# Performance work log

Hardware: AMD Instinct MI355X
Metric: run time of the kernel (lower is better)

The kernel has to match this reference:

```python
import jax, jax.numpy as jnp
import numpy as np

B, T, H, V = 128, 256, 1024, 4096


def setup_inputs() -> dict:
    key = jax.random.key(0)
    ks = jax.random.split(key, 11)
    s = 1.0 / np.sqrt(H)  # PyTorch default RNN/Linear init scale

    def u(k, shape):
        return jax.random.uniform(k, shape, jnp.float32, -s, s)

    return {
        "x": jax.random.normal(ks[0], (B, 1, T), jnp.float32),
        "W_ih0": u(ks[1], (H, 1)),
        "W_hh0": u(ks[2], (H, H)),
        "b_ih0": u(ks[3], (H,)),
        "b_hh0": u(ks[4], (H,)),
        "W_ih1": u(ks[5], (H, H)),
        "W_hh1": u(ks[6], (H, H)),
        "b_ih1": u(ks[7], (H,)),
        "b_hh1": u(ks[8], (H,)),
        "W_fc": u(ks[9], (V, H)),
        "b_fc": u(ks[10], (V,)),
        "text_length": B,
    }


def reference(x, W_ih0, W_hh0, b_ih0, b_hh0, W_ih1, W_hh1, b_ih1, b_hh1, W_fc, b_fc, text_length):
    # x: [B, 1, T] -> per-step scalar inputs xs: [T, B, 1]
    xs = jnp.transpose(x[:, 0, :], (1, 0))[:, :, None]
    h0 = jnp.zeros((text_length, W_hh0.shape[0]), x.dtype)
    h1 = jnp.zeros_like(h0)

    def step(carry, xt):
        h0, h1 = carry
        # 2-layer Elman RNN cell (tanh), one timestep
        h0n = jnp.tanh(xt @ W_ih0.T + b_ih0 + h0 @ W_hh0.T + b_hh0)
        h1n = jnp.tanh(h0n @ W_ih1.T + b_ih1 + h1 @ W_hh1.T + b_hh1)
        out = h1n @ W_fc.T + b_fc  # fused trailing linear, [B, V]
        return (h0n, h1n), out

    (h0, h1), outs = jax.lax.scan(step, (h0, h1), xs)  # outs: [T, B, V]
    # original returns cat over time then permute(1,0,2) -> [B, T, V]
    return jnp.transpose(outs, (1, 0, 2)), jnp.stack([h0, h1], axis=0)
```

## Files before the change

### kernel.cpp

```cpp
#include <hip/hip_runtime.h>

#define T_STEPS 256
#define BATCH   128
#define HDIM    1024
#define VDIM    4096
#define BH      (BATCH * HDIM)

typedef _Float16 half8 __attribute__((ext_vector_type(8)));
typedef _Float16 half4 __attribute__((ext_vector_type(4)));
typedef float    floatx4 __attribute__((ext_vector_type(4)));

__device__ __forceinline__ half8 ld_h8(const _Float16* p) { return *(const half8*)p; }

__device__ __forceinline__ void async16(void* l, const void* g) {
  __builtin_amdgcn_global_load_lds(
      (const __attribute__((address_space(1))) unsigned int*)g,
      (__attribute__((address_space(3))) unsigned int*)l, 16, 0, 0);
}

__device__ __forceinline__ void wait_ge(unsigned* f, unsigned tgt) {
  while (__hip_atomic_load(f, __ATOMIC_RELAXED, __HIP_MEMORY_SCOPE_AGENT) < tgt)
    __builtin_amdgcn_s_sleep(2);
  (void)__hip_atomic_load(f, __ATOMIC_ACQUIRE, __HIP_MEMORY_SCOPE_AGENT);
}
__device__ __forceinline__ void signal_inc(unsigned* f) {
  __hip_atomic_fetch_add(f, 1u, __ATOMIC_RELEASE, __HIP_MEMORY_SCOPE_AGENT);
}

__device__ __forceinline__ half8 lds_frag(const char* base, int row, int w) {
  return *(const half8*)(base + row * 2048 + ((w ^ (row & 7)) << 4));
}

__global__ __launch_bounds__(256) void f32_to_f16_kernel(
    const float* __restrict__ in, _Float16* __restrict__ out, int n4) {
  int i = blockIdx.x * 256 + threadIdx.x;
  if (i < n4) {
    float4 v = ((const float4*)in)[i];
    half4 h;
    h[0] = (_Float16)v.x; h[1] = (_Float16)v.y;
    h[2] = (_Float16)v.z; h[3] = (_Float16)v.w;
    ((half4*)out)[i] = h;
  }
}

__global__ __launch_bounds__(256, 1) void rnn_kernel(
    const float* __restrict__ x,
    const float* __restrict__ Wih0,
    const float* __restrict__ bih0, const float* __restrict__ bhh0,
    const float* __restrict__ bih1, const float* __restrict__ bhh1,
    const _Float16* __restrict__ W0h,
    const _Float16* __restrict__ W1i,
    const _Float16* __restrict__ W1h,
    _Float16* __restrict__ h0buf,
    _Float16* __restrict__ h1h,
    float* __restrict__ outh,
    unsigned* __restrict__ cnt0,
    unsigned* __restrict__ cnt1) {
  __shared__ __align__(16) char smem[65536];
  const int tid  = threadIdx.x;
  const int wv   = tid >> 6;
  const int lane = tid & 63;
  const int l15  = lane & 15;
  const int q    = lane >> 4;

  const int bid   = blockIdx.x;
  const int layer = bid >> 7;
  const int sub   = bid & 127;
  const int rg    = sub & 7;
  const int cg    = sub >> 3;
  const int rowbase = rg * 16;
  const int j     = cg * 64 + wv * 16 + l15;
  const int qe    = q * 8;

  if (layer == 0) {
    half8 w0r[32];
#pragma unroll
    for (int m = 0; m < 32; ++m)
      w0r[m] = ld_h8(W0h + (size_t)j * HDIM + m * 32 + qe);
    const float wih = Wih0[j];
    const float bb  = bih0[j] + bhh0[j];
    float* lx = (float*)(smem + 32768);
#pragma unroll
    for (int it = 0; it < 16; ++it)
      lx[it * 256 + tid] = x[rowbase * T_STEPS + it * 256 + tid];
    __syncthreads();

    for (int p = 0; p < T_STEPS; ++p) {
      if (tid == 0) {
        if (p >= 1) wait_ge(cnt0 + (((rg << 8) | (p - 1)) << 2), 16u);
        if (p >= 2) wait_ge(cnt1 + (((rg << 8) | (p - 2)) << 2), 16u);
      }
      __syncthreads();

      const _Float16* Ag = h0buf + (size_t)((p + 1) & 1) * BH + rowbase * HDIM;
#pragma unroll
      for (int it = 0; it < 8; ++it) {
        int c = it * 256 + tid;
        int row = c >> 7, cr = c & 127;
        async16(smem + it * 4096 + wv * 1024,
                Ag + row * HDIM + ((cr ^ (row & 7)) << 3));
      }
      asm volatile("s_waitcnt vmcnt(0)" ::: "memory");
      __syncthreads();

      floatx4 acc0 = {0.f, 0.f, 0.f, 0.f}, acc1 = {0.f, 0.f, 0.f, 0.f};
#pragma unroll
      for (int t = 0; t < 16; ++t) {
        acc0 = __builtin_amdgcn_mfma_f32_16x16x32_f16(
            lds_frag(smem, l15, 4 * t + q), w0r[t], acc0, 0, 0, 0);
        acc1 = __builtin_amdgcn_mfma_f32_16x16x32_f16(
            lds_frag(smem, l15, 64 + 4 * t + q), w0r[16 + t], acc1, 0, 0, 0);
      }
      floatx4 z = acc0 + acc1;
      _Float16* D = h0buf + (size_t)(p & 1) * BH;
#pragma unroll
      for (int r = 0; r < 4; ++r) {
        int b = rowbase + q * 4 + r;
        float h = tanhf(z[r] + lx[(q * 4 + r) * 256 + p] * wih + bb);
        D[b * HDIM + j] = (_Float16)h;
        if (p == T_STEPS - 1) outh[b * HDIM + j] = h;
      }
      asm volatile("s_waitcnt vmcnt(0)" ::: "memory");
      __syncthreads();
      if (tid == 0) signal_inc(cnt0 + (((rg << 8) | p) << 2));
    }
  } else {
    half8 w1r[32], w2r[32];
#pragma unroll
    for (int m = 0; m < 32; ++m) {
      w1r[m] = ld_h8(W1i + (size_t)j * HDIM + m * 32 + qe);
      w2r[m] = ld_h8(W1h + (size_t)j * HDIM + m * 32 + qe);
    }
    const float bb = bih1[j] + bhh1[j];

    for (int i = 0; i < T_STEPS; ++i) {
      if (tid == 0) {
        wait_ge(cnt0 + (((rg << 8) | i) << 2), 16u);
        if (i >= 1) wait_ge(cnt1 + (((rg << 8) | (i - 1)) << 2), 16u);
      }
      __syncthreads();

      const _Float16* A1 = h0buf + (size_t)(i & 1) * BH + rowbase * HDIM;
      const _Float16* A2 = h1h + (size_t)i * BH + rowbase * HDIM;
#pragma unroll
      for (int it = 0; it < 8; ++it) {
        int c = it * 256 + tid;
        int row = c >> 7, cr = c & 127;
        int so = row * HDIM + ((cr ^ (row & 7)) << 3);
        async16(smem + it * 4096 + wv * 1024, A1 + so);
        async16(smem + 32768 + it * 4096 + wv * 1024, A2 + so);
      }
      asm volatile("s_waitcnt vmcnt(0)" ::: "memory");
      __syncthreads();

      floatx4 a00 = {0.f,0.f,0.f,0.f}, a01 = {0.f,0.f,0.f,0.f};
      floatx4 a10 = {0.f,0.f,0.f,0.f}, a11 = {0.f,0.f,0.f,0.f};
#pragma unroll
      for (int t = 0; t < 16; ++t) {
        a00 = __builtin_amdgcn_mfma_f32_16x16x32_f16(
            lds_frag(smem, l15, 4 * t + q),              w1r[t],      a00, 0, 0, 0);
        a01 = __builtin_amdgcn_mfma_f32_16x16x32_f16(
            lds_frag(smem, l15, 64 + 4 * t + q),         w1r[16 + t], a01, 0, 0, 0);
        a10 = __builtin_amdgcn_mfma_f32_16x16x32_f16(
            lds_frag(smem + 32768, l15, 4 * t + q),      w2r[t],      a10, 0, 0, 0);
        a11 = __builtin_amdgcn_mfma_f32_16x16x32_f16(
            lds_frag(smem + 32768, l15, 64 + 4 * t + q), w2r[16 + t], a11, 0, 0, 0);
      }
      floatx4 z = (a00 + a01) + (a10 + a11);
      _Float16* D = h1h + (size_t)(i + 1) * BH;
#pragma unroll
      for (int r = 0; r < 4; ++r) {
        int b = rowbase + q * 4 + r;
        float h = tanhf(z[r] + bb);
        D[b * HDIM + j] = (_Float16)h;
        if (i == T_STEPS - 1) outh[BH + b * HDIM + j] = h;
      }
      asm volatile("s_waitcnt vmcnt(0)" ::: "memory");
      __syncthreads();
      if (tid == 0) signal_inc(cnt1 + (((rg << 8) | i) << 2));
    }
  }
}

__global__ __launch_bounds__(256) void fc_kernel(
    const _Float16* __restrict__ A,
    const _Float16* __restrict__ Wfc,
    const float* __restrict__ bfc,
    float* __restrict__ out) {
  __shared__ __align__(16) _Float16 As[128 * 64];
  __shared__ __align__(16) _Float16 Bs[128 * 64];
  const int tid  = threadIdx.x;
  const int wv   = tid >> 6;
  const int lane = tid & 63;
  const int l15  = lane & 15;
  const int q    = lane >> 4;
  const int t    = blockIdx.y;
  const int vt   = blockIdx.x;

  const _Float16* Ag = A   + (size_t)t * BH;
  const _Float16* Bg = Wfc + (size_t)vt * 128 * HDIM;

  floatx4 acc[4][4];
#pragma unroll
  for (int i = 0; i < 4; ++i)
#pragma unroll
    for (int jj = 0; jj < 4; ++jj) { floatx4 zz = {0.f,0.f,0.f,0.f}; acc[i][jj] = zz; }

  const int rowoff = (wv >> 1) * 64;
  const int coloff = (wv & 1) * 64;
  const int wbase  = wv * 1024;

  for (int kk = 0; kk < HDIM; kk += 64) {
#pragma unroll
    for (int r = 0; r < 4; ++r) {
      int c   = r * 256 + tid;
      int row = c >> 3;
      int gch = ((c & 7) ^ (row & 7)) << 3;
      async16((char*)As + r * 4096 + wbase, Ag + row * HDIM + kk + gch);
      async16((char*)Bs + r * 4096 + wbase, Bg + row * HDIM + kk + gch);
    }
    __syncthreads();
#pragma unroll
    for (int k2 = 0; k2 < 64; k2 += 32) {
      half8 af[4], bf[4];
      const int w = (k2 >> 3) + q;
#pragma unroll
      for (int i = 0; i < 4; ++i) {
        int rA = rowoff + i * 16 + l15;
        af[i] = *(const half8*)&As[rA * 64 + ((w ^ (rA & 7)) << 3)];
        int rB = coloff + i * 16 + l15;
        bf[i] = *(const half8*)&Bs[rB * 64 + ((w ^ (rB & 7)) << 3)];
      }
#pragma unroll
      for (int i = 0; i < 4; ++i)
#pragma unroll
        for (int jj = 0; jj < 4; ++jj)
          acc[i][jj] = __builtin_amdgcn_mfma_f32_16x16x32_f16(af[i], bf[jj], acc[i][jj], 0, 0, 0);
    }
    __syncthreads();
  }

#pragma unroll
  for (int i = 0; i < 4; ++i) {
    int b0 = rowoff + i * 16 + q * 4;
#pragma unroll
    for (int jj = 0; jj < 4; ++jj) {
      int v = vt * 128 + coloff + jj * 16 + l15;
      float bias = bfc[v];
#pragma unroll
      for (int r = 0; r < 4; ++r) {
        long o = (long)(b0 + r) * (T_STEPS * VDIM) + (long)t * VDIM + v;
        out[o] = acc[i][jj][r] + bias;
      }
    }
  }
}

extern "C" void kernel_launch(void* const* d_in, const int* in_sizes, int n_in,
                              void* d_out, int out_size, void* d_ws, size_t ws_size,
                              hipStream_t stream) {
  const float* x    = (const float*)d_in[0];
  const float* Wih0 = (const float*)d_in[1];
  const float* Whh0 = (const float*)d_in[2];
  const float* bih0 = (const float*)d_in[3];
  const float* bhh0 = (const float*)d_in[4];
  const float* Wih1 = (const float*)d_in[5];
  const float* Whh1 = (const float*)d_in[6];
  const float* bih1 = (const float*)d_in[7];
  const float* bhh1 = (const float*)d_in[8];
  const float* Wfc  = (const float*)d_in[9];
  const float* bfc  = (const float*)d_in[10];

  char* w = (char*)d_ws;
  _Float16* h0buf = (_Float16*)(w + 256);
  _Float16* h1h   = (_Float16*)(w + 256 + 2 * BH * 2);
  size_t off = 256 + (size_t)2 * BH * 2 + (size_t)(T_STEPS + 1) * BH * 2;
  _Float16* W0h16 = (_Float16*)(w + off); off += (size_t)HDIM * HDIM * 2;
  _Float16* W1i16 = (_Float16*)(w + off); off += (size_t)HDIM * HDIM * 2;
  _Float16* W1h16 = (_Float16*)(w + off); off += (size_t)HDIM * HDIM * 2;
  _Float16* Wfc16 = (_Float16*)(w + off); off += (size_t)VDIM * HDIM * 2;

  unsigned* cnt0 = (unsigned*)d_out;
  unsigned* cnt1 = cnt0 + 8192;
  hipMemsetAsync(d_out, 0, 65536, stream);
  hipMemsetAsync((void*)(h0buf + BH), 0, (size_t)2 * BH * 2, stream);

  f32_to_f16_kernel<<<(HDIM * HDIM / 4 + 255) / 256, 256, 0, stream>>>(Whh0, W0h16, HDIM * HDIM / 4);
  f32_to_f16_kernel<<<(HDIM * HDIM / 4 + 255) / 256, 256, 0, stream>>>(Wih1, W1i16, HDIM * HDIM / 4);
  f32_to_f16_kernel<<<(HDIM * HDIM / 4 + 255) / 256, 256, 0, stream>>>(Whh1, W1h16, HDIM * HDIM / 4);
  f32_to_f16_kernel<<<(VDIM * HDIM / 4 + 255) / 256, 256, 0, stream>>>(Wfc, Wfc16, VDIM * HDIM / 4);

  float* outh = (float*)d_out + (size_t)BATCH * T_STEPS * VDIM;
  rnn_kernel<<<256, 256, 0, stream>>>(x, Wih0, bih0, bhh0, bih1, bhh1,
                                      W0h16, W1i16, W1h16, h0buf, h1h, outh,
                                      cnt0, cnt1);

  fc_kernel<<<dim3(32, 256), 256, 0, stream>>>(h1h + BH, Wfc16, bfc, (float*)d_out);
}
```

Baseline: 3.064 ms.

## Deepen h0 ring buffer to eight slots to decouple RNN layers

Layer-0 hidden states now go into an 8-slot ring buffer held in the output scratch region instead of a double buffer. Layer 0 can then run up to eight steps ahead of layer 1 before it must wait. The two dependency waits are split across different threads so they can spin at the same time. Hidden-state writes use nontemporal stores. The ring buffer lives in d_out space that the fc kernel later overwrites, so the fc kernel must run only after the RNN finishes.

```diff
diff --git a/kernel.cpp b/kernel.cpp
--- a/kernel.cpp
+++ b/kernel.cpp
@@ -5,6 +5,7 @@
 #define HDIM    1024
 #define VDIM    4096
 #define BH      (BATCH * HDIM)
+#define H0_SLOTS 8
 
 typedef _Float16 half8 __attribute__((ext_vector_type(8)));
 typedef _Float16 half4 __attribute__((ext_vector_type(4)));
@@ -86,13 +87,14 @@
     __syncthreads();
 
     for (int p = 0; p < T_STEPS; ++p) {
-      if (tid == 0) {
-        if (p >= 1) wait_ge(cnt0 + (((rg << 8) | (p - 1)) << 2), 16u);
-        if (p >= 2) wait_ge(cnt1 + (((rg << 8) | (p - 2)) << 2), 16u);
-      }
-      __syncthreads();
-
-      const _Float16* Ag = h0buf + (size_t)((p + 1) & 1) * BH + rowbase * HDIM;
+      if (tid == 0 && p >= 1)
+        wait_ge(cnt0 + (((rg << 8) | (p - 1)) << 2), 16u);
+      if (tid == 64 && p >= H0_SLOTS)
+        wait_ge(cnt1 + (((rg << 8) | (p - H0_SLOTS)) << 2), 16u);
+      __syncthreads();
+
+      const _Float16* Ag =
+          h0buf + (size_t)((p + H0_SLOTS - 1) & (H0_SLOTS - 1)) * BH + rowbase * HDIM;
 #pragma unroll
       for (int it = 0; it < 8; ++it) {
         int c = it * 256 + tid;
@@ -112,12 +114,12 @@
             lds_frag(smem, l15, 64 + 4 * t + q), w0r[16 + t], acc1, 0, 0, 0);
       }
       floatx4 z = acc0 + acc1;
-      _Float16* D = h0buf + (size_t)(p & 1) * BH;
+      _Float16* D = h0buf + (size_t)(p & (H0_SLOTS - 1)) * BH;
 #pragma unroll
       for (int r = 0; r < 4; ++r) {
         int b = rowbase + q * 4 + r;
         float h = tanhf(z[r] + lx[(q * 4 + r) * 256 + p] * wih + bb);
-        D[b * HDIM + j] = (_Float16)h;
+        __builtin_nontemporal_store((_Float16)h, &D[b * HDIM + j]);
         if (p == T_STEPS - 1) outh[b * HDIM + j] = h;
       }
       asm volatile("s_waitcnt vmcnt(0)" ::: "memory");
@@ -134,13 +136,14 @@
     const float bb = bih1[j] + bhh1[j];
 
     for (int i = 0; i < T_STEPS; ++i) {
-      if (tid == 0) {
+      if (tid == 0)
         wait_ge(cnt0 + (((rg << 8) | i) << 2), 16u);
-        if (i >= 1) wait_ge(cnt1 + (((rg << 8) | (i - 1)) << 2), 16u);
-      }
-      __syncthreads();
-
-      const _Float16* A1 = h0buf + (size_t)(i & 1) * BH + rowbase * HDIM;
+      if (tid == 64 && i >= 1)
+        wait_ge(cnt1 + (((rg << 8) | (i - 1)) << 2), 16u);
+      __syncthreads();
+
+      const _Float16* A1 =
+          h0buf + (size_t)(i & (H0_SLOTS - 1)) * BH + rowbase * HDIM;
       const _Float16* A2 = h1h + (size_t)i * BH + rowbase * HDIM;
 #pragma unroll
       for (int it = 0; it < 8; ++it) {
@@ -172,7 +175,7 @@
       for (int r = 0; r < 4; ++r) {
         int b = rowbase + q * 4 + r;
         float h = tanhf(z[r] + bb);
-        D[b * HDIM + j] = (_Float16)h;
+        __builtin_nontemporal_store((_Float16)h, &D[b * HDIM + j]);
         if (i == T_STEPS - 1) outh[BH + b * HDIM + j] = h;
       }
       asm volatile("s_waitcnt vmcnt(0)" ::: "memory");
@@ -272,7 +275,6 @@
   const float* bfc  = (const float*)d_in[10];
 
   char* w = (char*)d_ws;
-  _Float16* h0buf = (_Float16*)(w + 256);
   _Float16* h1h   = (_Float16*)(w + 256 + 2 * BH * 2);
   size_t off = 256 + (size_t)2 * BH * 2 + (size_t)(T_STEPS + 1) * BH * 2;
   _Float16* W0h16 = (_Float16*)(w + off); off += (size_t)HDIM * HDIM * 2;
@@ -282,8 +284,10 @@
 
   unsigned* cnt0 = (unsigned*)d_out;
   unsigned* cnt1 = cnt0 + 8192;
+  _Float16* h0buf = (_Float16*)((char*)d_out + 65536);
   hipMemsetAsync(d_out, 0, 65536, stream);
-  hipMemsetAsync((void*)(h0buf + BH), 0, (size_t)2 * BH * 2, stream);
+  hipMemsetAsync((void*)(h0buf + (size_t)(H0_SLOTS - 1) * BH), 0, (size_t)BH * 2, stream);
+  hipMemsetAsync((void*)h1h, 0, (size_t)BH * 2, stream);
 
   f32_to_f16_kernel<<<(HDIM * HDIM / 4 + 255) / 256, 256, 0, stream>>>(Whh0, W0h16, HDIM * HDIM / 4);
   f32_to_f16_kernel<<<(HDIM * HDIM / 4 + 255) / 256, 256, 0, stream>>>(Wih1, W1i16, HDIM * HDIM / 4);
```

After: 3.331 ms. 1.09x slower.
